# Optimization experiments

Hardware: AMD Instinct MI355X
Metric: run time of the kernel (lower is better)

The kernel has to match this reference:

```python
import jax, jax.numpy as jnp
import numpy as np

B, M, C = 8, 1024, 768


def setup_inputs() -> dict:
    key = jax.random.key(0)
    ks = jax.random.split(key, 10)
    s = 0.02
    return {
        "layout_x": jax.random.normal(ks[0], (B, M, C), jnp.float32),
        "text_x": jax.random.normal(ks[1], (B, M, C), jnp.float32),
        "mask": jax.random.randint(ks[2], (B, M), 0, 2).astype(jnp.float32),
        "Wqkv": jax.random.normal(ks[3], (C, 3 * C), jnp.float32) * s,
        "bqkv": jnp.zeros((3 * C,), jnp.float32),
        "Wq": jax.random.normal(ks[4], (C, C), jnp.float32) * s,
        "bq": jnp.zeros((C,), jnp.float32),
        "Wkv": jax.random.normal(ks[5], (C, 2 * C), jnp.float32) * s,
        "bkv": jnp.zeros((2 * C,), jnp.float32),
        "Wffn": jax.random.normal(ks[6], (C, C), jnp.float32) * s,
        "bffn": jnp.zeros((C,), jnp.float32),
    }


def _masked_attn(q, k, v, pair_mask, scale):
    # pair_mask: [B,M,M] True where valid (mask_i * mask_j != 0)
    scores = jnp.einsum("bmd,bnd->bmn", q, k) * scale  # [B,M,M]
    scores = jnp.where(pair_mask, scores, jnp.float32(-10000.0))
    attn = jax.nn.softmax(scores, axis=-1)
    return jnp.einsum("bmn,bnd->bmd", attn, v)


def reference(layout_x, text_x, mask, Wqkv, bqkv, Wq, bq, Wkv, bkv, Wffn, bffn):
    dim = layout_x.shape[-1]
    scale = dim ** (-0.5)
    # mask repeated over C then mask@mask.T / C  ==  outer product of 1D masks
    pair = (mask[:, :, None] * mask[:, None, :]) != 0  # [B,M,M] bool, True=keep

    # self-attention on layout_x
    qkv = layout_x @ Wqkv + bqkv  # [B,M,3C]
    q, k, v = jnp.split(qkv, 3, axis=-1)
    layout_o = _masked_attn(q, k, v, pair, scale)

    # cross-attention: q from layout output, k/v from text_x
    cq = layout_o @ Wq + bq
    kv = text_x @ Wkv + bkv  # [B,M,2C]
    ck, cv = jnp.split(kv, 2, axis=-1)
    merge = _masked_attn(cq, ck, cv, pair, scale)

    return merge @ Wffn + bffn
```

## Files before the change

### kernel.cpp

```cpp
#include <hip/hip_runtime.h>
#include <math.h>

#define BDIM 8
#define MDIM 1024
#define CDIM 768
#define ROWS (BDIM * MDIM)

typedef __attribute__((ext_vector_type(8))) short short8;
typedef __attribute__((ext_vector_type(8))) unsigned short ushort8;
typedef __attribute__((ext_vector_type(4))) float f32x4;

#define MFMA16(a, b, c) __builtin_amdgcn_mfma_f32_16x16x32_bf16((a), (b), (c), 0, 0, 0)

#define BAR() __builtin_amdgcn_s_barrier()
#define FENCE() asm volatile("" ::: "memory")
#define SCHED_FENCE() __builtin_amdgcn_sched_barrier(0)
#define WAIT_LGKM0() asm volatile("s_waitcnt lgkmcnt(0)" ::: "memory")
#define WAIT_VM6() asm volatile("s_waitcnt vmcnt(6)" ::: "memory")
#define WAIT_VM0() asm volatile("s_waitcnt vmcnt(0)" ::: "memory")

__device__ __forceinline__ unsigned short f2bf(float f) {
  unsigned u = __float_as_uint(f);
  return (unsigned short)((u + 0x7FFFu + ((u >> 16) & 1u)) >> 16);
}

__global__ __launch_bounds__(256) void prologue(
    const float* __restrict__ xl, const float* __restrict__ xt,
    unsigned short* __restrict__ dxl, unsigned short* __restrict__ dxt,
    const float* __restrict__ W0, const float* __restrict__ W1,
    const float* __restrict__ W2, const float* __restrict__ W3,
    unsigned short* __restrict__ D0, unsigned short* __restrict__ D1,
    unsigned short* __restrict__ D2, unsigned short* __restrict__ D3) {
  const int bx = blockIdx.x;
  const int tid = threadIdx.x;
  if (bx < 6144) {
    const float* src = bx < 3072 ? xl : xt;
    unsigned short* dst = bx < 3072 ? dxl : dxt;
    const int i = ((bx < 3072 ? bx : bx - 3072) * 256 + tid) * 8;
    const float4 a = *(const float4*)(src + i);
    const float4 b = *(const float4*)(src + i + 4);
    ushort8 o;
    o[0] = f2bf(a.x); o[1] = f2bf(a.y); o[2] = f2bf(a.z); o[3] = f2bf(a.w);
    o[4] = f2bf(b.x); o[5] = f2bf(b.y); o[6] = f2bf(b.z); o[7] = f2bf(b.w);
    *(ushort8*)(dst + i) = o;
  } else {
    int x = bx - 6144;
    int bxx = x % 168;
    const int k0 = (x / 168) * 32;
    const float* W; unsigned short* D; int N;
    if (bxx < 72)       { W = W0; D = D0; N = 2304; }
    else if (bxx < 96)  { W = W1; D = D1; N = 768;  bxx -= 72; }
    else if (bxx < 144) { W = W2; D = D2; N = 1536; bxx -= 96; }
    else                { W = W3; D = D3; N = 768;  bxx -= 144; }
    __shared__ unsigned short t[32][33];
    const int tx = tid & 31, ty = tid >> 5;
    const int n0 = bxx * 32;
#pragma unroll
    for (int i = 0; i < 4; ++i)
      t[ty + i * 8][tx] = f2bf(W[(size_t)(k0 + ty + i * 8) * N + n0 + tx]);
    __syncthreads();
#pragma unroll
    for (int i = 0; i < 4; ++i)
      D[(size_t)(n0 + ty + i * 8) * CDIM + k0 + tx] = t[tx][ty + i * 8];
  }
}

__device__ __forceinline__ void stage64(
    const unsigned short* __restrict__ g, int ld, int k0,
    unsigned short* lds, int wave, int lane) {
  const int gchunk = (lane & 7) ^ (lane >> 3);
#pragma unroll
  for (int j = 0; j < 4; ++j) {
    const int grp = wave * 4 + j;
    const unsigned short* gp =
        g + (size_t)(grp * 8 + (lane >> 3)) * ld + k0 + gchunk * 8;
    __builtin_amdgcn_global_load_lds(
        (const __attribute__((address_space(1))) unsigned int*)gp,
        (__attribute__((address_space(3))) unsigned int*)(lds + grp * 512),
        16, 0, 0);
  }
}

__device__ __forceinline__ void mfma_loop64(
    const unsigned short* __restrict__ A, int lda,
    const unsigned short* __restrict__ Bt, int ldb, int K,
    unsigned short* As, unsigned short* Bs, f32x4 acc[4][4],
    int wave, int lane) {
  const int wx = wave & 1, wy = wave >> 1;
  const int quad = lane >> 4, l16 = lane & 15;
  for (int k0 = 0; k0 < K; k0 += 64) {
    stage64(A, lda, k0, As, wave, lane);
    stage64(Bt, ldb, k0, Bs, wave, lane);
    __syncthreads();
#pragma unroll
    for (int h = 0; h < 2; ++h) {
      const int slot = ((((h << 2) | quad) ^ (l16 & 7))) * 8;
      short8 afr[4], bfr[4];
#pragma unroll
      for (int mt = 0; mt < 4; ++mt)
        afr[mt] = *(const short8*)&As[(wy * 64 + mt * 16 + l16) * 64 + slot];
#pragma unroll
      for (int nt = 0; nt < 4; ++nt)
        bfr[nt] = *(const short8*)&Bs[(wx * 64 + nt * 16 + l16) * 64 + slot];
#pragma unroll
      for (int mt = 0; mt < 4; ++mt)
#pragma unroll
        for (int nt = 0; nt < 4; ++nt)
          acc[mt][nt] = MFMA16(afr[mt], bfr[nt], acc[mt][nt]);
    }
    __syncthreads();
  }
}

__device__ __forceinline__ void proj_epilogue(
    f32x4 acc[4][4], const float* __restrict__ bias,
    unsigned short* __restrict__ Y, unsigned short* __restrict__ vTd,
    int c0, int m0, int lastSlice, int trans, int wave, int lane) {
  const int wx = wave & 1, wy = wave >> 1;
  const int quad = lane >> 4, l16 = lane & 15;
  const int slice = c0 / 768;
  if (trans && slice == lastSlice) {
#pragma unroll
    for (int mt = 0; mt < 4; ++mt) {
      const int row0 = m0 + wy * 64 + mt * 16 + quad * 4;
      const int b = row0 >> 10, n0 = row0 & 1023;
#pragma unroll
      for (int nt = 0; nt < 4; ++nt) {
        const int gcol = c0 + wx * 64 + nt * 16 + l16;
        const int d = gcol - slice * 768;
        const float bv = bias[gcol];
        uint2 o;
        o.x = (unsigned)f2bf(acc[mt][nt][0] + bv) |
              ((unsigned)f2bf(acc[mt][nt][1] + bv) << 16);
        o.y = (unsigned)f2bf(acc[mt][nt][2] + bv) |
              ((unsigned)f2bf(acc[mt][nt][3] + bv) << 16);
        *(uint2*)&vTd[((size_t)b * CDIM + d) * MDIM + n0] = o;
      }
    }
  } else {
    const size_t sbase = (size_t)slice * ROWS * 768;
#pragma unroll
    for (int mt = 0; mt < 4; ++mt)
#pragma unroll
      for (int nt = 0; nt < 4; ++nt) {
        const int gcol = c0 + wx * 64 + nt * 16 + l16;
        const int lcol = gcol - slice * 768;
        const float bv = bias[gcol];
#pragma unroll
        for (int rg = 0; rg < 4; ++rg) {
          const int row = m0 + wy * 64 + mt * 16 + quad * 4 + rg;
          Y[sbase + (size_t)row * 768 + lcol] = f2bf(acc[mt][nt][rg] + bv);
        }
      }
  }
}

__device__ __forceinline__ void swizzle_mc(int lin, int* m0, int* c0) {
  const int xcd = lin & 7, j = lin >> 3;
  *m0 = (xcd * 8 + (j & 7)) * 128;
  *c0 = (j >> 3) * 128;
}

__device__ __forceinline__ void stage_half256(
    const unsigned short* __restrict__ g, int k0,
    unsigned short* lds, int wave, int lane) {
  const int gchunk = (lane & 7) ^ (lane >> 3);
#pragma unroll
  for (int j = 0; j < 2; ++j) {
    const int grp = wave * 2 + j;
    const unsigned short* gp =
        g + (size_t)(grp * 8 + (lane >> 3)) * CDIM + k0 + gchunk * 8;
    __builtin_amdgcn_global_load_lds(
        (const __attribute__((address_space(1))) unsigned int*)gp,
        (__attribute__((address_space(3))) unsigned int*)(lds + grp * 512),
        16, 0, 0);
  }
}

__device__ __forceinline__ void read_fragsA(
    const unsigned short* h, int roff, short8 fr[4][2], int l16, int quad) {
#pragma unroll
  for (int mf = 0; mf < 4; ++mf)
#pragma unroll
    for (int kh = 0; kh < 2; ++kh) {
      const int slot = (((kh << 2) | quad) ^ (l16 & 7)) * 8;
      fr[mf][kh] = *(const short8*)&h[(roff + mf * 16 + l16) * 64 + slot];
    }
}

__device__ __forceinline__ void read_fragsB(
    const unsigned short* h, int roff, short8 fr[2][2], int l16, int quad) {
#pragma unroll
  for (int nf = 0; nf < 2; ++nf)
#pragma unroll
    for (int kh = 0; kh < 2; ++kh) {
      const int slot = (((kh << 2) | quad) ^ (l16 & 7)) * 8;
      fr[nf][kh] = *(const short8*)&h[(roff + nf * 16 + l16) * 64 + slot];
    }
}

#define MFMA_PHASE(GM, GN, BB)                                              \
  do {                                                                      \
    SCHED_FENCE();                                                          \
    __builtin_amdgcn_s_setprio(1);                                          \
    _Pragma("unroll") for (int mf = 0; mf < 4; ++mf)                        \
    _Pragma("unroll") for (int nf = 0; nf < 2; ++nf)                        \
    _Pragma("unroll") for (int kh = 0; kh < 2; ++kh)                        \
        acc[GM][GN][mf][nf] =                                               \
            MFMA16(afr[mf][kh], BB[nf][kh], acc[GM][GN][mf][nf]);           \
    __builtin_amdgcn_s_setprio(0);                                          \
    SCHED_FENCE();                                                          \
  } while (0)

__global__ __launch_bounds__(512, 2) void gemm_qkvkv(
    const unsigned short* __restrict__ A0g, const unsigned short* __restrict__ B0g,
    const float* __restrict__ bias0, unsigned short* __restrict__ Y0,
    unsigned short* __restrict__ vT0,
    const unsigned short* __restrict__ A1g, const unsigned short* __restrict__ B1g,
    const float* __restrict__ bias1, unsigned short* __restrict__ Y1,
    unsigned short* __restrict__ vT1) {
  __shared__ __align__(16) unsigned short lds[65536];
  int lin = blockIdx.x;
  const unsigned short *A, *Bt; const float* bias;
  unsigned short *Y, *vTd; int lastSlice, m0, c0;
  if (lin < 288) {
    A = A0g; Bt = B0g; bias = bias0; Y = Y0; vTd = vT0; lastSlice = 2;
    const int xcd = lin & 7, j = lin >> 3;
    m0 = (xcd * 4 + (j & 3)) * 256; c0 = (j >> 2) * 256;
  } else {
    lin -= 288;
    A = A1g; Bt = B1g; bias = bias1; Y = Y1; vTd = vT1; lastSlice = 1;
    const int xcd = lin & 7, j = lin >> 3;
    m0 = (xcd * 4 + (j & 3)) * 256; c0 = (j >> 2) * 256;
  }
  const int tid = threadIdx.x;
  const int wave = tid >> 6, lane = tid & 63;
  const int wy = wave >> 2, wx = wave & 3;
  const int quad = lane >> 4, l16 = lane & 15;

  const unsigned short* Ah[2] = {A + (size_t)m0 * CDIM,
                                 A + (size_t)(m0 + 128) * CDIM};
  const unsigned short* Bh[2] = {Bt + (size_t)c0 * CDIM,
                                 Bt + (size_t)(c0 + 128) * CDIM};

  const f32x4 vzero = {0.f, 0.f, 0.f, 0.f};
  f32x4 acc[2][2][4][2];
#pragma unroll
  for (int gm = 0; gm < 2; ++gm)
#pragma unroll
    for (int gn = 0; gn < 2; ++gn)
#pragma unroll
      for (int mf = 0; mf < 4; ++mf)
#pragma unroll
        for (int nf = 0; nf < 2; ++nf) acc[gm][gn][mf][nf] = vzero;
  short8 afr[4][2], b0r[2][2], b1r[2][2];

  stage_half256(Ah[0], 0, lds + 0, wave, lane);
  stage_half256(Bh[0], 0, lds + 16384, wave, lane);
  stage_half256(Bh[1], 0, lds + 24576, wave, lane);
  stage_half256(Ah[1], 0, lds + 8192, wave, lane);
  stage_half256(Ah[0], 64, lds + 32768 + 0, wave, lane);
  stage_half256(Bh[0], 64, lds + 32768 + 16384, wave, lane);
  stage_half256(Bh[1], 64, lds + 32768 + 24576, wave, lane);
  WAIT_VM6();
  BAR(); FENCE();

  for (int t = 0; t < 12; ++t) {
    unsigned short* bufc = lds + (t & 1) * 32768;
    unsigned short* bufn = lds + ((t + 1) & 1) * 32768;
    read_fragsA(bufc + 0, wy * 64, afr, l16, quad);
    read_fragsB(bufc + 16384, wx * 32, b0r, l16, quad);
    if (t < 11) stage_half256(Ah[1], (t + 1) * 64, bufn + 8192, wave, lane);
    BAR(); WAIT_LGKM0();
    MFMA_PHASE(0, 0, b0r);
    read_fragsB(bufc + 24576, wx * 32, b1r, l16, quad);
    BAR(); WAIT_LGKM0();
    MFMA_PHASE(0, 1, b1r);
    read_fragsA(bufc + 8192, wy * 64, afr, l16, quad);
    if (t < 10) stage_half256(Ah[0], (t + 2) * 64, bufc + 0, wave, lane);
    BAR(); WAIT_LGKM0();
    MFMA_PHASE(1, 0, b0r);
    if (t < 10) {
      stage_half256(Bh[0], (t + 2) * 64, bufc + 16384, wave, lane);
      stage_half256(Bh[1], (t + 2) * 64, bufc + 24576, wave, lane);
      WAIT_VM6();
    } else if (t == 10) {
      WAIT_VM0();
    }
    BAR(); FENCE();
    MFMA_PHASE(1, 1, b1r);
  }

#pragma unroll
  for (int gm = 0; gm < 2; ++gm)
#pragma unroll
    for (int gn = 0; gn < 2; ++gn) {
      const int cb2 = c0 + gn * 128 + wx * 32;
      const int slice = cb2 / 768;
      const int rb = m0 + gm * 128 + wy * 64;
      if (slice == lastSlice) {
#pragma unroll
        for (int mf = 0; mf < 4; ++mf) {
          const int row0 = rb + mf * 16 + quad * 4;
          const int b = row0 >> 10, n0 = row0 & 1023;
#pragma unroll
          for (int nf = 0; nf < 2; ++nf) {
            const int gcol = cb2 + nf * 16 + l16;
            const int d = gcol - slice * 768;
            const float bv = bias[gcol];
            uint2 o;
            o.x = (unsigned)f2bf(acc[gm][gn][mf][nf][0] + bv) |
                  ((unsigned)f2bf(acc[gm][gn][mf][nf][1] + bv) << 16);
            o.y = (unsigned)f2bf(acc[gm][gn][mf][nf][2] + bv) |
                  ((unsigned)f2bf(acc[gm][gn][mf][nf][3] + bv) << 16);
            *(uint2*)&vTd[((size_t)b * CDIM + d) * MDIM + n0] = o;
          }
        }
      } else {
        const size_t sbase = (size_t)slice * ROWS * 768;
#pragma unroll
        for (int mf = 0; mf < 4; ++mf)
#pragma unroll
          for (int nf = 0; nf < 2; ++nf) {
            const int gcol = cb2 + nf * 16 + l16;
            const int lcol = gcol - slice * 768;
            const float bv = bias[gcol];
#pragma unroll
            for (int rg = 0; rg < 4; ++rg) {
              const int row = rb + mf * 16 + quad * 4 + rg;
              Y[sbase + (size_t)row * 768 + lcol] =
                  f2bf(acc[gm][gn][mf][nf][rg] + bv);
            }
          }
      }
    }
}

__global__ __launch_bounds__(256, 4) void gemm_proj(
    const unsigned short* __restrict__ A, const unsigned short* __restrict__ Bt,
    const float* __restrict__ bias, unsigned short* __restrict__ Y,
    unsigned short* __restrict__ vTd, int trans) {
  __shared__ __align__(16) unsigned short As[128 * 64];
  __shared__ __align__(16) unsigned short Bs[128 * 64];
  int m0, c0;
  swizzle_mc(blockIdx.y * gridDim.x + blockIdx.x, &m0, &c0);
  const int tid = threadIdx.x;
  const int wave = tid >> 6, lane = tid & 63;
  const f32x4 vzero = {0.f, 0.f, 0.f, 0.f};
  f32x4 acc[4][4];
#pragma unroll
  for (int mt = 0; mt < 4; ++mt)
#pragma unroll
    for (int nt = 0; nt < 4; ++nt) acc[mt][nt] = vzero;
  mfma_loop64(A + (size_t)m0 * CDIM, CDIM, Bt + (size_t)c0 * CDIM, CDIM, CDIM,
              As, Bs, acc, wave, lane);
  proj_epilogue(acc, bias, Y, vTd, c0, m0, (int)(gridDim.x / 6) - 1, trans,
                wave, lane);
}

__global__ __launch_bounds__(256, 4) void gemm_ffn(
    const unsigned short* __restrict__ A, const unsigned short* __restrict__ Bt,
    const float* __restrict__ bias, float* __restrict__ Y) {
  __shared__ __align__(16) unsigned short As[128 * 64];
  __shared__ __align__(16) unsigned short Bs[128 * 64];
  int m0, c0;
  swizzle_mc(blockIdx.y * gridDim.x + blockIdx.x, &m0, &c0);
  const int tid = threadIdx.x;
  const int wave = tid >> 6, lane = tid & 63;
  const int wx = wave & 1, wy = wave >> 1;
  const int quad = lane >> 4, l16 = lane & 15;
  const f32x4 vzero = {0.f, 0.f, 0.f, 0.f};
  f32x4 acc[4][4];
#pragma unroll
  for (int mt = 0; mt < 4; ++mt)
#pragma unroll
    for (int nt = 0; nt < 4; ++nt) acc[mt][nt] = vzero;
  mfma_loop64(A + (size_t)m0 * CDIM, CDIM, Bt + (size_t)c0 * CDIM, CDIM, CDIM,
              As, Bs, acc, wave, lane);
#pragma unroll
  for (int mt = 0; mt < 4; ++mt)
#pragma unroll
    for (int nt = 0; nt < 4; ++nt) {
      const int col = c0 + wx * 64 + nt * 16 + l16;
      const float bv = bias[col];
#pragma unroll
      for (int rg = 0; rg < 4; ++rg) {
        const int row = m0 + wy * 64 + mt * 16 + quad * 4 + rg;
        Y[(size_t)row * 768 + col] = acc[mt][nt][rg] + bv;
      }
    }
}

__global__ __launch_bounds__(256, 4) void gemm_qk(
    const unsigned short* __restrict__ Qb, const unsigned short* __restrict__ Kb,
    const float* __restrict__ mask, unsigned short* __restrict__ S, float scale,
    float* __restrict__ rsp) {
  __shared__ __align__(16) unsigned short As[128 * 64];
  __shared__ __align__(16) unsigned short Bs[128 * 64];
  const int c0 = blockIdx.x * 128;
  const int m0 = blockIdx.y * 128;
  const int b = blockIdx.z;
  const int tid = threadIdx.x;
  const int wave = tid >> 6, lane = tid & 63;
  const int wx = wave & 1, wy = wave >> 1;
  const int quad = lane >> 4, l16 = lane & 15;

  const f32x4 vzero = {0.f, 0.f, 0.f, 0.f};
  f32x4 acc[4][4];
#pragma unroll
  for (int mt = 0; mt < 4; ++mt)
#pragma unroll
    for (int nt = 0; nt < 4; ++nt) acc[mt][nt] = vzero;

  mfma_loop64(Qb + ((size_t)b * MDIM + m0) * CDIM, CDIM,
              Kb + ((size_t)b * MDIM + c0) * CDIM, CDIM, CDIM,
              As, Bs, acc, wave, lane);

  const float* maskb = mask + b * MDIM;
  float mrow[4][4], rsum[4][4];
#pragma unroll
  for (int mt = 0; mt < 4; ++mt)
#pragma unroll
    for (int rg = 0; rg < 4; ++rg) {
      mrow[mt][rg] = maskb[m0 + wy * 64 + mt * 16 + quad * 4 + rg];
      rsum[mt][rg] = 0.f;
    }
  unsigned short* Sb = S + (size_t)b * MDIM * MDIM;
#pragma unroll
  for (int nt = 0; nt < 4; ++nt) {
    const int col = c0 + wx * 64 + nt * 16 + l16;
    const float mcol = maskb[col];
#pragma unroll
    for (int mt = 0; mt < 4; ++mt)
#pragma unroll
      for (int rg = 0; rg < 4; ++rg) {
        const int row = m0 + wy * 64 + mt * 16 + quad * 4 + rg;
        const float e = (mrow[mt][rg] * mcol != 0.f)
                            ? __expf(acc[mt][nt][rg] * scale)
                            : 1e-30f;
        Sb[(size_t)row * MDIM + col] = f2bf(e);
        rsum[mt][rg] += e;
      }
  }
  for (int off = 1; off < 16; off <<= 1) {
#pragma unroll
    for (int mt = 0; mt < 4; ++mt)
#pragma unroll
      for (int rg = 0; rg < 4; ++rg)
        rsum[mt][rg] += __shfl_xor(rsum[mt][rg], off, 64);
  }
  if (l16 == 0) {
    float* rs = rsp + ((((size_t)blockIdx.x * 2 + wx) * 8 + b) << 10) +
                m0 + wy * 64;
#pragma unroll
    for (int mt = 0; mt < 4; ++mt)
#pragma unroll
      for (int rg = 0; rg < 4; ++rg)
        rs[mt * 16 + quad * 4 + rg] = rsum[mt][rg];
  }
}

__global__ __launch_bounds__(256, 4) void attn_pv(
    const unsigned short* __restrict__ P, const unsigned short* __restrict__ vT,
    unsigned short* __restrict__ O, const float* __restrict__ rsp) {
  __shared__ __align__(16) unsigned short As[128 * 64];
  __shared__ __align__(16) unsigned short Bs[128 * 64];
  const int c0 = blockIdx.x * 128;
  const int m0 = blockIdx.y * 128;
  const int b = blockIdx.z;
  const int tid = threadIdx.x;
  const int wave = tid >> 6, lane = tid & 63;
  const int wx = wave & 1, wy = wave >> 1;
  const int quad = lane >> 4, l16 = lane & 15;

  const f32x4 vzero = {0.f, 0.f, 0.f, 0.f};
  f32x4 acc[4][4];
#pragma unroll
  for (int mt = 0; mt < 4; ++mt)
#pragma unroll
    for (int nt = 0; nt < 4; ++nt) acc[mt][nt] = vzero;

  mfma_loop64(P + ((size_t)b * MDIM + m0) * MDIM, MDIM,
              vT + ((size_t)b * CDIM + c0) * MDIM, MDIM, MDIM,
              As, Bs, acc, wave, lane);

  const float* rsb = rsp + (((size_t)l16 * 8 + b) << 10) + m0 + wy * 64;
  float inv[4][4];
#pragma unroll
  for (int mt = 0; mt < 4; ++mt)
#pragma unroll
    for (int rg = 0; rg < 4; ++rg) {
      float s = rsb[mt * 16 + quad * 4 + rg];
      for (int off = 1; off < 16; off <<= 1) s += __shfl_xor(s, off, 64);
      inv[mt][rg] = 1.f / s;
    }
#pragma unroll
  for (int mt = 0; mt < 4; ++mt)
#pragma unroll
    for (int nt = 0; nt < 4; ++nt)
#pragma unroll
      for (int rg = 0; rg < 4; ++rg) {
        const int row = m0 + wy * 64 + mt * 16 + quad * 4 + rg;
        const int col = c0 + wx * 64 + nt * 16 + l16;
        O[(size_t)(b * MDIM + row) * CDIM + col] =
            f2bf(acc[mt][nt][rg] * inv[mt][rg]);
      }
}

extern "C" void kernel_launch(void* const* d_in, const int* in_sizes, int n_in,
                              void* d_out, int out_size, void* d_ws, size_t ws_size,
                              hipStream_t stream) {
  const float* layout_x = (const float*)d_in[0];
  const float* text_x   = (const float*)d_in[1];
  const float* maskp    = (const float*)d_in[2];
  const float* Wqkv     = (const float*)d_in[3];
  const float* bqkv     = (const float*)d_in[4];
  const float* Wq       = (const float*)d_in[5];
  const float* bq       = (const float*)d_in[6];
  const float* Wkv      = (const float*)d_in[7];
  const float* bkv      = (const float*)d_in[8];
  const float* Wffn     = (const float*)d_in[9];
  const float* bffn     = (const float*)d_in[10];
  float* out = (float*)d_out;
  char* ws = (char*)d_ws;

  const float scale = 1.0f / sqrtf((float)CDIM);

  unsigned short* xlb    = (unsigned short*)(ws);
  unsigned short* xtb    = (unsigned short*)(ws + 12582912);
  unsigned short* Wqkv_t = (unsigned short*)(ws + 25165824);
  unsigned short* Wq_t   = (unsigned short*)(ws + 28704768);
  unsigned short* Wkv_t  = (unsigned short*)(ws + 29884416);
  unsigned short* Wffn_t = (unsigned short*)(ws + 32243712);
  unsigned short* Qb     = (unsigned short*)(ws + 33423360);
  unsigned short* Kb     = (unsigned short*)(ws + 46006272);
  unsigned short* vT     = (unsigned short*)(ws + 58589184);
  unsigned short* S      = (unsigned short*)(ws + 71172096);
  unsigned short* attn1  = xlb;
  unsigned short* cqb    = Qb;
  unsigned short* cK  = (unsigned short*)out;
  unsigned short* cVT = (unsigned short*)out + 6291456;
  float* rsp = (float*)xtb;

  prologue<<<10176, 256, 0, stream>>>(layout_x, text_x, xlb, xtb,
                                      Wqkv, Wq, Wkv, Wffn,
                                      Wqkv_t, Wq_t, Wkv_t, Wffn_t);
  gemm_qkvkv<<<480, 512, 0, stream>>>(xlb, Wqkv_t, bqkv, Qb, vT,
                                      xtb, Wkv_t, bkv, cK, cVT);
  gemm_qk<<<dim3(8, 8, BDIM), 256, 0, stream>>>(Qb, Kb, maskp, S, scale, rsp);
  attn_pv<<<dim3(6, 8, BDIM), 256, 0, stream>>>(S, vT, attn1, rsp);
  gemm_proj<<<dim3(6, 64), 256, 0, stream>>>(attn1, Wq_t, bq, cqb, vT, 0);
  gemm_qk<<<dim3(8, 8, BDIM), 256, 0, stream>>>(cqb, cK, maskp, S, scale, rsp);
  attn_pv<<<dim3(6, 8, BDIM), 256, 0, stream>>>(S, cVT, attn1, rsp);
  gemm_ffn<<<dim3(6, 64), 256, 0, stream>>>(attn1, Wffn_t, bffn, out);
}
```

Measured before the change: 311.8 us.

## Software-pipeline LDS fragment reads across MFMA phases in QKV GEMM

```diff
diff --git a/kernel.cpp b/kernel.cpp
--- a/kernel.cpp
+++ b/kernel.cpp
@@ -16,7 +16,12 @@
 #define FENCE() asm volatile("" ::: "memory")
 #define SCHED_FENCE() __builtin_amdgcn_sched_barrier(0)
 #define WAIT_LGKM0() asm volatile("s_waitcnt lgkmcnt(0)" ::: "memory")
+#define WAIT_LGKM4() asm volatile("s_waitcnt lgkmcnt(4)" ::: "memory")
+#define WAIT_LGKM8() asm volatile("s_waitcnt lgkmcnt(8)" ::: "memory")
+#define WAIT_VM8() asm volatile("s_waitcnt vmcnt(8)" ::: "memory")
 #define WAIT_VM6() asm volatile("s_waitcnt vmcnt(6)" ::: "memory")
+#define WAIT_VM4() asm volatile("s_waitcnt vmcnt(4)" ::: "memory")
+#define WAIT_VM2() asm volatile("s_waitcnt vmcnt(2)" ::: "memory")
 #define WAIT_VM0() asm volatile("s_waitcnt vmcnt(0)" ::: "memory")
 
 __device__ __forceinline__ unsigned short f2bf(float f) {
@@ -199,7 +204,7 @@
     }
 }
 
-#define MFMA_PHASE(GM, GN, BB)                                              \
+#define MFMA_PHASE(GM, GN, AA, BB)                                          \
   do {                                                                      \
     SCHED_FENCE();                                                          \
     __builtin_amdgcn_s_setprio(1);                                          \
@@ -207,7 +212,7 @@
     _Pragma("unroll") for (int nf = 0; nf < 2; ++nf)                        \
     _Pragma("unroll") for (int kh = 0; kh < 2; ++kh)                        \
         acc[GM][GN][mf][nf] =                                               \
-            MFMA16(afr[mf][kh], BB[nf][kh], acc[GM][GN][mf][nf]);           \
+            MFMA16(AA[mf][kh], BB[nf][kh], acc[GM][GN][mf][nf]);            \
     __builtin_amdgcn_s_setprio(0);                                          \
     SCHED_FENCE();                                                          \
   } while (0)
@@ -253,7 +258,7 @@
       for (int mf = 0; mf < 4; ++mf)
 #pragma unroll
         for (int nf = 0; nf < 2; ++nf) acc[gm][gn][mf][nf] = vzero;
-  short8 afr[4][2], b0r[2][2], b1r[2][2];
+  short8 afrE[4][2], afrO[4][2], b0r[2][2], b1r[2][2];
 
   stage_half256(Ah[0], 0, lds + 0, wave, lane);
   stage_half256(Bh[0], 0, lds + 16384, wave, lane);
@@ -262,33 +267,64 @@
   stage_half256(Ah[0], 64, lds + 32768 + 0, wave, lane);
   stage_half256(Bh[0], 64, lds + 32768 + 16384, wave, lane);
   stage_half256(Bh[1], 64, lds + 32768 + 24576, wave, lane);
-  WAIT_VM6();
+  WAIT_VM8();
   BAR(); FENCE();
-
-  for (int t = 0; t < 12; ++t) {
+  read_fragsA(lds + 0, wy * 64, afrE, l16, quad);
+  read_fragsB(lds + 16384, wx * 32, b0r, l16, quad);
+
+  for (int t = 0; t < 10; ++t) {
     unsigned short* bufc = lds + (t & 1) * 32768;
     unsigned short* bufn = lds + ((t + 1) & 1) * 32768;
-    read_fragsA(bufc + 0, wy * 64, afr, l16, quad);
-    read_fragsB(bufc + 16384, wx * 32, b0r, l16, quad);
-    if (t < 11) stage_half256(Ah[1], (t + 1) * 64, bufn + 8192, wave, lane);
-    BAR(); WAIT_LGKM0();
-    MFMA_PHASE(0, 0, b0r);
     read_fragsB(bufc + 24576, wx * 32, b1r, l16, quad);
-    BAR(); WAIT_LGKM0();
-    MFMA_PHASE(0, 1, b1r);
-    read_fragsA(bufc + 8192, wy * 64, afr, l16, quad);
-    if (t < 10) stage_half256(Ah[0], (t + 2) * 64, bufc + 0, wave, lane);
-    BAR(); WAIT_LGKM0();
-    MFMA_PHASE(1, 0, b0r);
-    if (t < 10) {
-      stage_half256(Bh[0], (t + 2) * 64, bufc + 16384, wave, lane);
-      stage_half256(Bh[1], (t + 2) * 64, bufc + 24576, wave, lane);
-      WAIT_VM6();
-    } else if (t == 10) {
-      WAIT_VM0();
-    }
-    BAR(); FENCE();
-    MFMA_PHASE(1, 1, b1r);
+    stage_half256(Ah[1], (t + 1) * 64, bufn + 8192, wave, lane);
+    WAIT_VM8(); BAR(); WAIT_LGKM4();
+    MFMA_PHASE(0, 0, afrE, b0r);
+    read_fragsA(bufc + 8192, wy * 64, afrO, l16, quad);
+    stage_half256(Ah[0], (t + 2) * 64, bufc + 0, wave, lane);
+    WAIT_VM8(); BAR(); WAIT_LGKM8();
+    MFMA_PHASE(0, 1, afrE, b1r);
+    read_fragsA(bufn + 0, wy * 64, afrE, l16, quad);
+    stage_half256(Bh[0], (t + 2) * 64, bufc + 16384, wave, lane);
+    WAIT_VM8(); BAR(); WAIT_LGKM8();
+    MFMA_PHASE(1, 0, afrO, b0r);
+    read_fragsB(bufn + 16384, wx * 32, b0r, l16, quad);
+    stage_half256(Bh[1], (t + 2) * 64, bufc + 24576, wave, lane);
+    WAIT_VM8(); BAR(); WAIT_LGKM4();
+    MFMA_PHASE(1, 1, afrO, b1r);
+  }
+  {
+    unsigned short* bufc = lds + 0;
+    unsigned short* bufn = lds + 32768;
+    read_fragsB(bufc + 24576, wx * 32, b1r, l16, quad);
+    stage_half256(Ah[1], 11 * 64, bufn + 8192, wave, lane);
+    WAIT_VM8(); BAR(); WAIT_LGKM4();
+    MFMA_PHASE(0, 0, afrE, b0r);
+
+    read_fragsA(bufc + 8192, wy * 64, afrO, l16, quad);
+    WAIT_VM6(); BAR(); WAIT_LGKM8();
+    MFMA_PHASE(0, 1, afrE, b1r);
+
+    read_fragsA(bufn + 0, wy * 64, afrE, l16, quad);
+    WAIT_VM4(); BAR(); WAIT_LGKM8();
+    MFMA_PHASE(1, 0, afrO, b0r);
+
+    read_fragsB(bufn + 16384, wx * 32, b0r, l16, quad);
+    WAIT_VM2(); BAR(); WAIT_LGKM4();
+    MFMA_PHASE(1, 1, afrO, b1r);
+  }
+  {
+    unsigned short* bufc = lds + 32768;
+    read_fragsB(bufc + 24576, wx * 32, b1r, l16, quad);
+    WAIT_VM0(); BAR(); WAIT_LGKM4();
+    MFMA_PHASE(0, 0, afrE, b0r);
+
+    read_fragsA(bufc + 8192, wy * 64, afrO, l16, quad);
+    WAIT_LGKM8();
+    MFMA_PHASE(0, 1, afrE, b1r);
+
+    WAIT_LGKM0();
+    MFMA_PHASE(1, 0, afrO, b0r);
+    MFMA_PHASE(1, 1, afrO, b1r);
   }
 
 #pragma unroll
```

After: 311.7 us. About the same (-0.0%).
